# Kernel optimization log

Hardware: AMD Instinct MI355X
Metric: run time of the kernel (lower is better)

Reference implementation:

```python
import jax, jax.numpy as jnp
import numpy as np

B, T, H, D, O = 2, 2048, 16, 64, 1024  # batch, seq, heads, head_size, output_size
E = H * D


def setup_inputs() -> dict:
    key = jax.random.key(0)
    ks = jax.random.split(key, 8)
    return {
        "query": jax.random.normal(ks[0], (B, T, E), jnp.float32),
        "key": jax.random.normal(ks[1], (B, T, E), jnp.float32),
        "value": jax.random.normal(ks[2], (B, T, E), jnp.float32),
        "Wq": jax.random.normal(ks[3], (E, E), jnp.float32) * (E ** -0.5),
        "Wk": jax.random.normal(ks[4], (E, E), jnp.float32) * (E ** -0.5),
        "Wv": jax.random.normal(ks[5], (E, E), jnp.float32) * (E ** -0.5),
        "proj_kernel": jax.random.normal(ks[6], (H, D, O), jnp.float32) * (D ** -0.5),
        "proj_bias": jax.random.normal(ks[7], (O,), jnp.float32),
    }


def reference(query, key, value, Wq, Wk, Wv, proj_kernel, proj_bias):
    # Linear projections (torch nn.Linear: x @ W.T), then split heads
    q = (query @ Wq.T).reshape(B, T, H, D)
    k = (key @ Wk.T).reshape(B, T, H, D)
    v = (value @ Wv.T).reshape(B, T, H, D)
    q = q * (D ** -0.5)  # scale query by 1/sqrt(head_size)
    # logits: [B, H, N, M]
    logits = jnp.einsum("bnhd,bmhd->bhnm", q, k)
    attn_coef = jax.nn.softmax(logits, axis=-1)
    # attn @ V -> [B, N, H, D]
    mh = jnp.einsum("bhnm,bmhd->bnhd", attn_coef, v)
    # custom output projection with per-head kernel [H, D, O]
    out = jnp.einsum("bnhd,hdo->bno", mh, proj_kernel) + proj_bias
    return out, attn_coef
```

## Files before the change

kernel.cpp:

```cpp
#include <hip/hip_runtime.h>
#include <hip/hip_bf16.h>
#include <math.h>

#define B_ 2
#define T_ 2048
#define H_ 16
#define D_ 64
#define E_ 1024
#define O_ 1024
#define BT_ 4096
#define SCALE_Q 0.18033688011f

typedef __attribute__((ext_vector_type(8))) short bf8;
typedef __attribute__((ext_vector_type(4))) float f4;

static __device__ __forceinline__ unsigned short f2bf(float f) {
  unsigned u = __builtin_bit_cast(unsigned, f);
  u += 0x7FFFu + ((u >> 16) & 1u);
  return (unsigned short)(u >> 16);
}

static __device__ __forceinline__ unsigned cvtpk_bf(float lo, float hi) {
  unsigned r;
  asm("v_cvt_pk_bf16_f32 %0, %1, %2" : "=v"(r) : "v"(lo), "v"(hi));
  return r;
}

static __device__ __forceinline__ uint4 cvt8(float4 a, float4 b) {
  uint4 v;
  v.x = cvtpk_bf(a.x, a.y);
  v.y = cvtpk_bf(a.z, a.w);
  v.z = cvtpk_bf(b.x, b.y);
  v.w = cvtpk_bf(b.z, b.w);
  return v;
}

static __device__ __forceinline__ f4 mfma16(bf8 a, bf8 b, f4 c) {
  return __builtin_amdgcn_mfma_f32_16x16x32_bf16(a, b, c, 0, 0, 0);
}

static __device__ __forceinline__ float ex2(float x) {
  float r;
  asm("v_exp_f32 %0, %1" : "=v"(r) : "v"(x));
  return r;
}

__global__ __launch_bounds__(256) void qkv_gemm(const float* __restrict__ Xq,
                                                const float* __restrict__ Xk,
                                                const float* __restrict__ Xv,
                                                const float* __restrict__ Wq,
                                                const float* __restrict__ Wk,
                                                const float* __restrict__ Wv,
                                                unsigned short* __restrict__ dq,
                                                unsigned short* __restrict__ dk,
                                                unsigned short* __restrict__ dv) {
  __shared__ __align__(16) unsigned short lA[64 * 40];
  __shared__ __align__(16) unsigned short lB[128 * 40];
  const int z = blockIdx.z;
  const float* X = (z == 0) ? Xq : (z == 1) ? Xk : Xv;
  const float* W = (z == 0) ? Wq : (z == 1) ? Wk : Wv;
  unsigned short* dst = (z == 0) ? dq : (z == 1) ? dk : dv;
  const float scale = (z == 0) ? SCALE_Q : 1.0f;

  const int tid = threadIdx.x;
  const int bx = blockIdx.x, by = blockIdx.y;
  const int lane = tid & 63, w = tid >> 6;
  const int l15 = lane & 15, qd = lane >> 4;
  const int wr = (w >> 1) * 32, wc = (w & 1) * 64;

  const int ar = tid >> 2, akc = (tid & 3) << 3;
  const int br = tid >> 1, bkc = (tid & 1) << 4;
  const float* aptr = X + (size_t)(bx * 64 + ar) * E_ + akc;
  const float* bptr = W + (size_t)(by * 128 + br) * E_ + bkc;

  f4 acc[2][4];
#pragma unroll
  for (int i = 0; i < 2; ++i)
#pragma unroll
    for (int j = 0; j < 4; ++j) acc[i][j] = (f4){0.f, 0.f, 0.f, 0.f};

  for (int k0 = 0; k0 < E_; k0 += 32) {
    __syncthreads();
    {
      const float4* p = (const float4*)aptr;
      *(uint4*)&lA[ar * 40 + akc] = cvt8(p[0], p[1]);
    }
    {
      const float4* p = (const float4*)bptr;
      *(uint4*)&lB[br * 40 + bkc] = cvt8(p[0], p[1]);
      *(uint4*)&lB[br * 40 + bkc + 8] = cvt8(p[2], p[3]);
    }
    aptr += 32; bptr += 32;
    __syncthreads();

    bf8 af[2], bfr[4];
#pragma unroll
    for (int rt = 0; rt < 2; ++rt)
      af[rt] = *(const bf8*)&lA[(wr + rt * 16 + l15) * 40 + qd * 8];
#pragma unroll
    for (int ct = 0; ct < 4; ++ct)
      bfr[ct] = *(const bf8*)&lB[(wc + ct * 16 + l15) * 40 + qd * 8];
#pragma unroll
    for (int rt = 0; rt < 2; ++rt)
#pragma unroll
      for (int ct = 0; ct < 4; ++ct)
        acc[rt][ct] = mfma16(af[rt], bfr[ct], acc[rt][ct]);
  }

#pragma unroll
  for (int rt = 0; rt < 2; ++rt)
#pragma unroll
    for (int ct = 0; ct < 4; ++ct)
#pragma unroll
      for (int r = 0; r < 4; ++r) {
        int m = bx * 64 + wr + rt * 16 + qd * 4 + r;
        int n = by * 128 + wc + ct * 16 + l15;
        int b = m >> 11, t = m & 2047;
        int h = n >> 6, d = n & 63;
        dst[((size_t)(b * H_ + h) * T_ + t) * D_ + d] = f2bf(acc[rt][ct][r] * scale);
      }
}

__global__ __launch_bounds__(256) void transpose_all(const unsigned short* __restrict__ vh,
                                                     unsigned short* __restrict__ vt,
                                                     const float* __restrict__ pk,
                                                     unsigned short* __restrict__ pt) {
  __shared__ __align__(16) unsigned short lT[64 * 72];
  const int tid = threadIdx.x;
  if (blockIdx.x < 1024) {
    const int bh = blockIdx.x >> 5;
    const int t0 = (blockIdx.x & 31) * 64;
    const unsigned short* src = vh + (size_t)bh * T_ * D_ + (size_t)t0 * D_;
#pragma unroll
    for (int i = 0; i < 2; ++i) {
      int c = tid + i * 256;
      int row = c >> 3, dc = (c & 7) << 3;
      *(uint4*)&lT[row * 72 + dc] = *(const uint4*)(src + row * D_ + dc);
    }
    __syncthreads();
    unsigned short* dstp = vt + (size_t)bh * D_ * T_;
#pragma unroll
    for (int i = 0; i < 2; ++i) {
      int c = tid + i * 256;
      int d = c >> 3, tc = (c & 7) << 3;
      union { unsigned short s[8]; uint4 v; } u;
#pragma unroll
      for (int j = 0; j < 8; ++j) u.s[j] = lT[(tc + j) * 72 + d];
      *(uint4*)(dstp + (size_t)d * T_ + t0 + tc) = u.v;
    }
  } else {
    const int bx = blockIdx.x - 1024;
    const int hd0 = (bx >> 4) * 64;
    const int o0 = (bx & 15) * 64;
#pragma unroll
    for (int i = 0; i < 2; ++i) {
      int c = tid + i * 256;
      int row = c >> 3, oc = (c & 7) << 3;
      const float4* p = (const float4*)(pk + (size_t)(hd0 + row) * O_ + o0 + oc);
      *(uint4*)&lT[row * 72 + oc] = cvt8(p[0], p[1]);
    }
    __syncthreads();
#pragma unroll
    for (int i = 0; i < 2; ++i) {
      int c = tid + i * 256;
      int orow = c >> 3, hc = (c & 7) << 3;
      union { unsigned short s[8]; uint4 v; } u;
#pragma unroll
      for (int j = 0; j < 8; ++j) u.s[j] = lT[(hc + j) * 72 + orow];
      *(uint4*)(pt + (size_t)(o0 + orow) * E_ + hd0 + hc) = u.v;
    }
  }
}

__global__ __launch_bounds__(512) void attention(const unsigned short* __restrict__ qh,
                                                 const unsigned short* __restrict__ kh,
                                                 const unsigned short* __restrict__ vt,
                                                 float* __restrict__ attn,
                                                 unsigned short* __restrict__ mh) {
  __shared__ __align__(16) unsigned short lK[64 * 72];
  __shared__ __align__(16) unsigned short lV[64 * 72];
  __shared__ __align__(16) unsigned short lP[8 * 16 * 72];

  const int tid = threadIdx.x;
  const int bh = blockIdx.x >> 4;
  const int n0 = (blockIdx.x & 15) * 128;
  const int lane = tid & 63, w = tid >> 6;
  const int l15 = lane & 15, qd = lane >> 4;

  const unsigned short* qbase = qh + ((size_t)bh * T_ + n0) * D_;
  const unsigned short* kbase = kh + (size_t)bh * T_ * D_;
  const unsigned short* vbase = vt + (size_t)bh * D_ * T_;

  const bf8 aq0 = *(const bf8*)(qbase + (w * 16 + l15) * D_ + qd * 8);
  const bf8 aq1 = *(const bf8*)(qbase + (w * 16 + l15) * D_ + 32 + qd * 8);

  const int srow = tid >> 3, scol = (tid & 7) << 3;

  float mL = -INFINITY, lL = 0.f;
  for (int m0 = 0; m0 < T_; m0 += 64) {
    __syncthreads();
    *(uint4*)&lK[srow * 72 + scol] = *(const uint4*)(kbase + (size_t)(m0 + srow) * D_ + scol);
    __syncthreads();
    f4 s[4];
#pragma unroll
    for (int kk = 0; kk < 4; ++kk) {
      bf8 k0 = *(const bf8*)&lK[(kk * 16 + l15) * 72 + qd * 8];
      bf8 k1 = *(const bf8*)&lK[(kk * 16 + l15) * 72 + 32 + qd * 8];
      f4 t = (f4){0.f, 0.f, 0.f, 0.f};
      t = mfma16(k0, aq0, t);
      t = mfma16(k1, aq1, t);
      s[kk] = t;
    }
    float tm = s[0][0];
#pragma unroll
    for (int kk = 0; kk < 4; ++kk)
#pragma unroll
      for (int r = 0; r < 4; ++r) tm = fmaxf(tm, s[kk][r]);
    float nm = fmaxf(mL, tm);
    lL *= ex2(mL - nm);
    mL = nm;
#pragma unroll
    for (int kk = 0; kk < 4; ++kk)
#pragma unroll
      for (int r = 0; r < 4; ++r) lL += ex2(s[kk][r] - mL);
  }

  float mrow = mL, lrow = lL;
#pragma unroll
  for (int off = 16; off < 64; off <<= 1) {
    float om = __shfl_xor(mrow, off);
    float ol = __shfl_xor(lrow, off);
    float nm = fmaxf(mrow, om);
    lrow = lrow * ex2(mrow - nm) + ol * ex2(om - nm);
    mrow = nm;
  }
  const float invl = 1.0f / lrow;

  f4 o[4];
#pragma unroll
  for (int dt = 0; dt < 4; ++dt) o[dt] = (f4){0.f, 0.f, 0.f, 0.f};

  float* attnrow = attn + ((size_t)bh * T_ + n0 + w * 16 + l15) * T_ + qd * 4;
  unsigned short* lPw = lP + w * 16 * 72;

  for (int m0 = 0; m0 < T_; m0 += 64) {
    __syncthreads();
    *(uint4*)&lK[srow * 72 + scol] = *(const uint4*)(kbase + (size_t)(m0 + srow) * D_ + scol);
    *(uint4*)&lV[srow * 72 + scol] = *(const uint4*)(vbase + (size_t)srow * T_ + m0 + scol);
    __syncthreads();
    f4 s[4];
#pragma unroll
    for (int kk = 0; kk < 4; ++kk) {
      bf8 k0 = *(const bf8*)&lK[(kk * 16 + l15) * 72 + qd * 8];
      bf8 k1 = *(const bf8*)&lK[(kk * 16 + l15) * 72 + 32 + qd * 8];
      f4 t = (f4){0.f, 0.f, 0.f, 0.f};
      t = mfma16(k0, aq0, t);
      t = mfma16(k1, aq1, t);
      s[kk] = t;
    }
#pragma unroll
    for (int kk = 0; kk < 4; ++kk) {
      float p0 = ex2(s[kk][0] - mrow) * invl;
      float p1 = ex2(s[kk][1] - mrow) * invl;
      float p2 = ex2(s[kk][2] - mrow) * invl;
      float p3 = ex2(s[kk][3] - mrow) * invl;
      f4 pf = (f4){p0, p1, p2, p3};
      __builtin_nontemporal_store(pf, (f4*)(attnrow + m0 + kk * 16));
      uint2 pb;
      pb.x = cvtpk_bf(p0, p1);
      pb.y = cvtpk_bf(p2, p3);
      *(uint2*)&lPw[l15 * 72 + kk * 16 + qd * 4] = pb;
    }
    bf8 ap0 = *(const bf8*)&lPw[l15 * 72 + qd * 8];
    bf8 ap1 = *(const bf8*)&lPw[l15 * 72 + 32 + qd * 8];
#pragma unroll
    for (int dt = 0; dt < 4; ++dt) {
      bf8 bv0 = *(const bf8*)&lV[(dt * 16 + l15) * 72 + qd * 8];
      bf8 bv1 = *(const bf8*)&lV[(dt * 16 + l15) * 72 + 32 + qd * 8];
      o[dt] = mfma16(ap0, bv0, o[dt]);
      o[dt] = mfma16(ap1, bv1, o[dt]);
    }
  }

  const int b = bh >> 4, h = bh & 15;
#pragma unroll
  for (int dt = 0; dt < 4; ++dt)
#pragma unroll
    for (int r = 0; r < 4; ++r) {
      int t = n0 + w * 16 + qd * 4 + r;
      int d = dt * 16 + l15;
      mh[(size_t)(b * T_ + t) * E_ + h * D_ + d] = f2bf(o[dt][r]);
    }
}

__global__ __launch_bounds__(256) void out_gemm(const unsigned short* __restrict__ A,
                                                const unsigned short* __restrict__ Bm,
                                                const float* __restrict__ bias,
                                                float* __restrict__ Cout) {
  __shared__ __align__(16) unsigned short lA[64 * 40];
  __shared__ __align__(16) unsigned short lB[128 * 40];
  const int tid = threadIdx.x;
  const int bx = blockIdx.x, by = blockIdx.y;
  const int lane = tid & 63, w = tid >> 6;
  const int l15 = lane & 15, qd = lane >> 4;
  const int wr = (w >> 1) * 32, wc = (w & 1) * 64;

  const int ar = tid >> 2, akc = (tid & 3) << 3;
  const unsigned short* aptr = A + (size_t)(bx * 64 + ar) * E_ + akc;

  f4 acc[2][4];
#pragma unroll
  for (int i = 0; i < 2; ++i)
#pragma unroll
    for (int j = 0; j < 4; ++j) acc[i][j] = (f4){0.f, 0.f, 0.f, 0.f};

  for (int k0 = 0; k0 < E_; k0 += 32) {
    __syncthreads();
    *(uint4*)&lA[ar * 40 + akc] = *(const uint4*)aptr;
#pragma unroll
    for (int i = 0; i < 2; ++i) {
      int c = tid + i * 256;
      int br = c >> 2, bkc = (c & 3) << 3;
      *(uint4*)&lB[br * 40 + bkc] =
          *(const uint4*)(Bm + (size_t)(by * 128 + br) * E_ + k0 + bkc);
    }
    aptr += 32;
    __syncthreads();

    bf8 af[2], bfr[4];
#pragma unroll
    for (int rt = 0; rt < 2; ++rt)
      af[rt] = *(const bf8*)&lA[(wr + rt * 16 + l15) * 40 + qd * 8];
#pragma unroll
    for (int ct = 0; ct < 4; ++ct)
      bfr[ct] = *(const bf8*)&lB[(wc + ct * 16 + l15) * 40 + qd * 8];
#pragma unroll
    for (int rt = 0; rt < 2; ++rt)
#pragma unroll
      for (int ct = 0; ct < 4; ++ct)
        acc[rt][ct] = mfma16(af[rt], bfr[ct], acc[rt][ct]);
  }

#pragma unroll
  for (int ct = 0; ct < 4; ++ct) {
    int n = by * 128 + wc + ct * 16 + l15;
    float bv = bias[n];
#pragma unroll
    for (int rt = 0; rt < 2; ++rt)
#pragma unroll
      for (int r = 0; r < 4; ++r) {
        int m = bx * 64 + wr + rt * 16 + qd * 4 + r;
        __builtin_nontemporal_store(acc[rt][ct][r] + bv, &Cout[(size_t)m * O_ + n]);
      }
  }
}

extern "C" void kernel_launch(void* const* d_in, const int* in_sizes, int n_in,
                              void* d_out, int out_size, void* d_ws, size_t ws_size,
                              hipStream_t stream) {
  const float* query = (const float*)d_in[0];
  const float* key_i = (const float*)d_in[1];
  const float* value = (const float*)d_in[2];
  const float* Wq = (const float*)d_in[3];
  const float* Wk = (const float*)d_in[4];
  const float* Wv = (const float*)d_in[5];
  const float* pk = (const float*)d_in[6];
  const float* pb = (const float*)d_in[7];

  float* out = (float*)d_out;
  float* attn = out + (size_t)BT_ * O_;

  unsigned short* ws = (unsigned short*)d_ws;
  unsigned short* qh = ws;
  unsigned short* kh = qh + (size_t)4194304;
  unsigned short* vh = kh + (size_t)4194304;
  unsigned short* vtb = vh + (size_t)4194304;
  unsigned short* pt = vtb + (size_t)4194304;
  unsigned short* mhb = vh;

  dim3 blk(256, 1, 1);
  hipLaunchKernelGGL(qkv_gemm, dim3(64, 8, 3), blk, 0, stream,
                     query, key_i, value, Wq, Wk, Wv, qh, kh, vh);
  hipLaunchKernelGGL(transpose_all, dim3(1280), blk, 0, stream, vh, vtb, pk, pt);
  hipLaunchKernelGGL(attention, dim3(512), dim3(512, 1, 1), 0, stream, qh, kh, vtb, attn, mhb);
  hipLaunchKernelGGL(out_gemm, dim3(64, 8), blk, 0, stream, mhb, pt, pb, out);
}
```

Baseline: 817.8 us.

## Register-prefetch next tiles in GEMMs and attention, shrink attention blocks with swizzle

The QKV GEMM, output GEMM and both attention passes now load the next K-step tile into registers right after the barrier, so global loads overlap the MFMA work instead of stalling before each LDS store. Attention is relaunched with 256-thread blocks covering 64 query rows (1024 blocks), and each thread stages two K/V rows. A block-index swizzle spreads consecutive blocks across heads. This adds register pressure and one wasted wrap-around prefetch per loop.

```diff
diff --git a/kernel.cpp b/kernel.cpp
--- a/kernel.cpp
+++ b/kernel.cpp
@@ -70,8 +70,12 @@
 
   const int ar = tid >> 2, akc = (tid & 3) << 3;
   const int br = tid >> 1, bkc = (tid & 1) << 4;
-  const float* aptr = X + (size_t)(bx * 64 + ar) * E_ + akc;
-  const float* bptr = W + (size_t)(by * 128 + br) * E_ + bkc;
+  const float* abase = X + (size_t)(bx * 64 + ar) * E_ + akc;
+  const float* bbase = W + (size_t)(by * 128 + br) * E_ + bkc;
+
+  float4 pa0 = ((const float4*)abase)[0], pa1 = ((const float4*)abase)[1];
+  float4 pb0 = ((const float4*)bbase)[0], pb1 = ((const float4*)bbase)[1];
+  float4 pb2 = ((const float4*)bbase)[2], pb3 = ((const float4*)bbase)[3];
 
   f4 acc[2][4];
 #pragma unroll
@@ -81,17 +85,15 @@
 
   for (int k0 = 0; k0 < E_; k0 += 32) {
     __syncthreads();
-    {
-      const float4* p = (const float4*)aptr;
-      *(uint4*)&lA[ar * 40 + akc] = cvt8(p[0], p[1]);
-    }
-    {
-      const float4* p = (const float4*)bptr;
-      *(uint4*)&lB[br * 40 + bkc] = cvt8(p[0], p[1]);
-      *(uint4*)&lB[br * 40 + bkc + 8] = cvt8(p[2], p[3]);
-    }
-    aptr += 32; bptr += 32;
-    __syncthreads();
+    *(uint4*)&lA[ar * 40 + akc] = cvt8(pa0, pa1);
+    *(uint4*)&lB[br * 40 + bkc] = cvt8(pb0, pb1);
+    *(uint4*)&lB[br * 40 + bkc + 8] = cvt8(pb2, pb3);
+    __syncthreads();
+
+    const int kn = (k0 + 32) & (E_ - 1);
+    pa0 = ((const float4*)(abase + kn))[0]; pa1 = ((const float4*)(abase + kn))[1];
+    pb0 = ((const float4*)(bbase + kn))[0]; pb1 = ((const float4*)(bbase + kn))[1];
+    pb2 = ((const float4*)(bbase + kn))[2]; pb3 = ((const float4*)(bbase + kn))[3];
 
     bf8 af[2], bfr[4];
 #pragma unroll
@@ -172,18 +174,19 @@
   }
 }
 
-__global__ __launch_bounds__(512) void attention(const unsigned short* __restrict__ qh,
+__global__ __launch_bounds__(256) void attention(const unsigned short* __restrict__ qh,
                                                  const unsigned short* __restrict__ kh,
                                                  const unsigned short* __restrict__ vt,
                                                  float* __restrict__ attn,
                                                  unsigned short* __restrict__ mh) {
   __shared__ __align__(16) unsigned short lK[64 * 72];
   __shared__ __align__(16) unsigned short lV[64 * 72];
-  __shared__ __align__(16) unsigned short lP[8 * 16 * 72];
+  __shared__ __align__(16) unsigned short lP[4 * 16 * 72];
 
   const int tid = threadIdx.x;
-  const int bh = blockIdx.x >> 4;
-  const int n0 = (blockIdx.x & 15) * 128;
+  const int swz = (blockIdx.x & 7) * 128 + (blockIdx.x >> 3);
+  const int bh = swz >> 5;
+  const int n0 = (swz & 31) * 64;
   const int lane = tid & 63, w = tid >> 6;
   const int l15 = lane & 15, qd = lane >> 4;
 
@@ -195,12 +198,19 @@
   const bf8 aq1 = *(const bf8*)(qbase + (w * 16 + l15) * D_ + 32 + qd * 8);
 
   const int srow = tid >> 3, scol = (tid & 7) << 3;
-
+  const unsigned short* kst = kbase + (size_t)srow * D_ + scol;
+
+  uint4 kr0 = *(const uint4*)kst;
+  uint4 kr1 = *(const uint4*)(kst + 32 * D_);
   float mL = -INFINITY, lL = 0.f;
   for (int m0 = 0; m0 < T_; m0 += 64) {
     __syncthreads();
-    *(uint4*)&lK[srow * 72 + scol] = *(const uint4*)(kbase + (size_t)(m0 + srow) * D_ + scol);
-    __syncthreads();
+    *(uint4*)&lK[srow * 72 + scol] = kr0;
+    *(uint4*)&lK[(srow + 32) * 72 + scol] = kr1;
+    __syncthreads();
+    const int mn = (m0 + 64) & (T_ - 1);
+    kr0 = *(const uint4*)(kst + (size_t)mn * D_);
+    kr1 = *(const uint4*)(kst + (size_t)(mn + 32) * D_);
     f4 s[4];
 #pragma unroll
     for (int kk = 0; kk < 4; ++kk) {
@@ -242,12 +252,26 @@
 
   float* attnrow = attn + ((size_t)bh * T_ + n0 + w * 16 + l15) * T_ + qd * 4;
   unsigned short* lPw = lP + w * 16 * 72;
+  const unsigned short* vst = vbase + (size_t)srow * T_ + scol;
+
+  kr0 = *(const uint4*)kst;
+  kr1 = *(const uint4*)(kst + 32 * D_);
+  uint4 vr0 = *(const uint4*)vst;
+  uint4 vr1 = *(const uint4*)(vst + 32 * T_);
 
   for (int m0 = 0; m0 < T_; m0 += 64) {
     __syncthreads();
-    *(uint4*)&lK[srow * 72 + scol] = *(const uint4*)(kbase + (size_t)(m0 + srow) * D_ + scol);
-    *(uint4*)&lV[srow * 72 + scol] = *(const uint4*)(vbase + (size_t)srow * T_ + m0 + scol);
-    __syncthreads();
+    *(uint4*)&lK[srow * 72 + scol] = kr0;
+    *(uint4*)&lK[(srow + 32) * 72 + scol] = kr1;
+    *(uint4*)&lV[srow * 72 + scol] = vr0;
+    *(uint4*)&lV[(srow + 32) * 72 + scol] = vr1;
+    __syncthreads();
+    const int mn = (m0 + 64) & (T_ - 1);
+    kr0 = *(const uint4*)(kst + (size_t)mn * D_);
+    kr1 = *(const uint4*)(kst + (size_t)(mn + 32) * D_);
+    vr0 = *(const uint4*)(vst + mn);
+    vr1 = *(const uint4*)(vst + 32 * T_ + mn);
+
     f4 s[4];
 #pragma unroll
     for (int kk = 0; kk < 4; ++kk) {
@@ -306,7 +330,15 @@
   const int wr = (w >> 1) * 32, wc = (w & 1) * 64;
 
   const int ar = tid >> 2, akc = (tid & 3) << 3;
-  const unsigned short* aptr = A + (size_t)(bx * 64 + ar) * E_ + akc;
+  const unsigned short* abase = A + (size_t)(bx * 64 + ar) * E_ + akc;
+  const int br0 = tid >> 2, bkc0 = (tid & 3) << 3;
+  const int br1 = (tid + 256) >> 2, bkc1 = bkc0;
+  const unsigned short* bbase0 = Bm + (size_t)(by * 128 + br0) * E_ + bkc0;
+  const unsigned short* bbase1 = Bm + (size_t)(by * 128 + br1) * E_ + bkc1;
+
+  uint4 pa = *(const uint4*)abase;
+  uint4 pb0 = *(const uint4*)bbase0;
+  uint4 pb1 = *(const uint4*)bbase1;
 
   f4 acc[2][4];
 #pragma unroll
@@ -316,16 +348,14 @@
 
   for (int k0 = 0; k0 < E_; k0 += 32) {
     __syncthreads();
-    *(uint4*)&lA[ar * 40 + akc] = *(const uint4*)aptr;
-#pragma unroll
-    for (int i = 0; i < 2; ++i) {
-      int c = tid + i * 256;
-      int br = c >> 2, bkc = (c & 3) << 3;
-      *(uint4*)&lB[br * 40 + bkc] =
-          *(const uint4*)(Bm + (size_t)(by * 128 + br) * E_ + k0 + bkc);
-    }
-    aptr += 32;
-    __syncthreads();
+    *(uint4*)&lA[ar * 40 + akc] = pa;
+    *(uint4*)&lB[br0 * 40 + bkc0] = pb0;
+    *(uint4*)&lB[br1 * 40 + bkc1] = pb1;
+    __syncthreads();
+    const int kn = (k0 + 32) & (E_ - 1);
+    pa = *(const uint4*)(abase + kn);
+    pb0 = *(const uint4*)(bbase0 + kn);
+    pb1 = *(const uint4*)(bbase1 + kn);
 
     bf8 af[2], bfr[4];
 #pragma unroll
@@ -382,6 +412,6 @@
   hipLaunchKernelGGL(qkv_gemm, dim3(64, 8, 3), blk, 0, stream,
                      query, key_i, value, Wq, Wk, Wv, qh, kh, vh);
   hipLaunchKernelGGL(transpose_all, dim3(1280), blk, 0, stream, vh, vtb, pk, pt);
-  hipLaunchKernelGGL(attention, dim3(512), dim3(512, 1, 1), 0, stream, qh, kh, vtb, attn, mhb);
+  hipLaunchKernelGGL(attention, dim3(1024), blk, 0, stream, qh, kh, vtb, attn, mhb);
   hipLaunchKernelGGL(out_gemm, dim3(64, 8), blk, 0, stream, mhb, pt, pb, out);
 }
```

Result: faster. 790.3 us (-3.4%).
